# Kernel optimization log

Measured on AMD Instinct MI355X. Metric: run time of the kernel, lower is better.

The kernel has to match this reference:

```python
import jax, jax.numpy as jnp
import numpy as np

B, T, M, P = 256, 128, 64, 64


def setup_inputs() -> dict:
    key = jax.random.key(0)
    ks = jax.random.split(key, 20)
    s = 0.05
    inp = {
        "data": jax.random.normal(ks[0], (B, T - 1, 1), jnp.float32),
        "encoder_h": jax.random.normal(ks[1], (B, T, M), jnp.float32),
        "h0": jax.random.normal(ks[2], (B, P), jnp.float32),
        "s0": jax.random.normal(ks[3], (B, P), jnp.float32),
        # dense: Dense(1) on concat([x, context]) -> in=1+M
        "W_dense": jax.random.normal(ks[4], (1 + M, 1), jnp.float32) * s,
        "b_dense": jnp.zeros((1,), jnp.float32),
        # LSTM(p): kernel (1,4p), recurrent (p,4p), bias (4p); keras gate order i,f,c,o
        "Wk": jax.random.normal(ks[5], (1, 4 * P), jnp.float32) * s,
        "Uk": jax.random.normal(ks[6], (P, 4 * P), jnp.float32) * s,
        "bk": jnp.zeros((4 * P,), jnp.float32),
        # temporal attention: W_d Dense(m) on concat([h,c]) (2p -> m)
        "Wd": jax.random.normal(ks[7], (2 * P, M), jnp.float32) * s,
        "bWd": jnp.zeros((M,), jnp.float32),
        # U_d Dense(m) on encoder_h (m -> m)
        "Ud": jax.random.normal(ks[8], (M, M), jnp.float32) * s,
        "bUd": jnp.zeros((M,), jnp.float32),
        # v_d Dense(1)
        "vd": jax.random.normal(ks[9], (M, 1), jnp.float32) * s,
        "bvd": jnp.zeros((1,), jnp.float32),
        # dense_vb: Dense(1) on concat([h, context]) (p+m -> 1)
        "Wvb": jax.random.normal(ks[10], (P + M, 1), jnp.float32) * s,
        "bvb": jnp.zeros((1,), jnp.float32),
        # dense_Wb: Dense(p) applied AFTER dense_vb (1 -> p), as in the source
        "Wb": jax.random.normal(ks[11], (1, P), jnp.float32) * s,
        "bWb": jnp.zeros((P,), jnp.float32),
    }
    return inp


def reference(data, encoder_h, h0, s0, W_dense, b_dense, Wk, Uk, bk,
              Wd, bWd, Ud, bUd, vd, bvd, Wvb, bvb, Wb, bWb):
    # Loop-invariant: U_d(encoder_h), (B,T,M). Math identical to per-step compute.
    Ue = jnp.einsum('btm,mn->btn', encoder_h, Ud) + bUd

    def step(carry, x_t):
        ctx, _h = carry                      # ctx: (B,M)
        inp = jnp.concatenate([x_t, ctx], axis=-1)   # (B, 1+M)
        y = inp @ W_dense + b_dense                   # (B,1)
        # NOTE: source resets LSTM state to (h0, s0) at every step.
        z = y @ Wk + h0 @ Uk + bk                     # (B,4P)
        i_g, f_g, g_g, o_g = jnp.split(z, 4, axis=-1)
        c = jax.nn.sigmoid(f_g) * s0 + jax.nn.sigmoid(i_g) * jnp.tanh(g_g)
        h = jax.nn.sigmoid(o_g) * jnp.tanh(c)         # (B,P)
        # temporal attention
        dproj = jnp.concatenate([h, c], axis=-1) @ Wd + bWd   # (B,M)
        e = jnp.tanh(dproj[:, None, :] + Ue) @ vd + bvd        # (B,T,1)
        beta = jax.nn.softmax(e, axis=1)                       # (B,T,1)
        ctx_new = jnp.einsum('bti,btm->bm', beta, encoder_h)   # (B,M)
        return (ctx_new, h), None

    Bsz = encoder_h.shape[0]
    carry0 = (jnp.zeros((Bsz, Wk.shape[1] // 4 * 0 + encoder_h.shape[2]), encoder_h.dtype),
              jnp.zeros((Bsz, Uk.shape[0]), encoder_h.dtype))
    xs = jnp.transpose(data, (1, 0, 2))  # (T-1, B, 1)
    (ctx, h), _ = jax.lax.scan(step, carry0, xs)

    concatenated = jnp.concatenate([h, ctx], axis=-1)[:, None, :]  # (B,1,P+M)
    out = (concatenated @ Wvb + bvb) @ Wb + bWb                     # (B,1,P)
    return out
```

## Files before the change

kernel.cpp:

```cpp
#include <hip/hip_runtime.h>


#define Bn 256
#define Tn 128
#define Mn 64
#define Pn 64
#define NTH 512
#define NW 8
#define UST 68
#define DPST 72
#define K2C 2.885390081777927f

__device__ __forceinline__ float fexp(float x) {
    return __builtin_amdgcn_exp2f(x * 1.44269504088896341f);
}
__device__ __forceinline__ float fexp2(float x) { return __builtin_amdgcn_exp2f(x); }
__device__ __forceinline__ float frcp(float x) { return __builtin_amdgcn_rcpf(x); }
__device__ __forceinline__ float fsig(float x) { return frcp(1.0f + fexp(-x)); }
__device__ __forceinline__ float ftanh(float x) { return 1.0f - 2.0f * frcp(1.0f + fexp(2.0f * x)); }

template <int CTRL>
__device__ __forceinline__ float dppmov(float x) {
    return __int_as_float(__builtin_amdgcn_update_dpp(
        0, __float_as_int(x), CTRL, 0xf, 0xf, false));
}
__device__ __forceinline__ float rdlane(float x, int l) {
    return __int_as_float(__builtin_amdgcn_readlane(__float_as_int(x), l));
}
__device__ __forceinline__ float wavesum(float x) {
    x += dppmov<0x111>(x);
    x += dppmov<0x112>(x);
    x += dppmov<0x114>(x);
    x += dppmov<0x118>(x);
    x += dppmov<0x142>(x);
    x += dppmov<0x143>(x);
    return rdlane(x, 63);
}

#define OFF_ENC   0
#define OFF_UD    8704
#define OFF_PRE   13056
#define OFF_DPART 13312
#define OFF_DPROJ 13888
#define OFF_ES    13952
#define OFF_CTXP  14080
#define OFF_YS    14592
#define OFF_XS    14600
#define SMEM_FLOATS 14728

__global__ __launch_bounds__(NTH, 1)
void decoder_kernel(const float* __restrict__ data, const float* __restrict__ enc,
                    const float* __restrict__ h0, const float* __restrict__ s0,
                    const float* __restrict__ W_dense, const float* __restrict__ b_dense,
                    const float* __restrict__ Wk, const float* __restrict__ Uk,
                    const float* __restrict__ bk,
                    const float* __restrict__ Wd, const float* __restrict__ bWd,
                    const float* __restrict__ Ud, const float* __restrict__ bUd,
                    const float* __restrict__ vd, const float* __restrict__ bvd,
                    const float* __restrict__ Wvb, const float* __restrict__ bvb,
                    const float* __restrict__ Wb, const float* __restrict__ bWb,
                    float* __restrict__ out)
{
    extern __shared__ float smem[];
    float* enc_s   = smem + OFF_ENC;
    float* Ud_s    = smem + OFF_UD;
    float* pre_s   = smem + OFF_PRE;
    float* dpart   = smem + OFF_DPART;
    float* dproj_s = smem + OFF_DPROJ;
    float* e_s     = smem + OFF_ES;
    float* ctxp    = smem + OFF_CTXP;
    float* ys_s    = smem + OFF_YS;
    float* x_s     = smem + OFF_XS;

    const int b    = blockIdx.x;
    const int tid  = threadIdx.x;
    const int lane = tid & 63;
    const int wv   = tid >> 6;

    {
        const float* encg = enc + (size_t)b * Tn * Mn;
        #pragma unroll
        for (int i = 0; i < 4; i++) {
            int flat = (i * NTH + tid) * 4;
            int t = flat >> 6, m = flat & 63;
            *(float4*)(enc_s + t * UST + m) = *(const float4*)(encg + flat);
        }
        #pragma unroll
        for (int i = 0; i < 2; i++) {
            int flat = (i * NTH + tid) * 4;
            int k = flat >> 6, n = flat & 63;
            *(float4*)(Ud_s + k * UST + n) = *(const float4*)(Ud + flat);
        }
        if (tid < Tn - 1) x_s[tid] = data[(size_t)b * (Tn - 1) + tid];
        if (tid < 4 * Pn) {
            float s = bk[tid];
            const float* h0b = h0 + b * Pn;
            #pragma unroll
            for (int k = 0; k < Pn; k++) s = fmaf(h0b[k], Uk[k * 4 * Pn + tid], s);
            pre_s[tid] = s;
        }
        if (tid < NW) ys_s[tid] = 0.0f;
        ctxp[tid] = 0.0f;
    }
    __syncthreads();

    const int t_e = tid >> 2, q_e = tid & 3, m0 = q_e * 16;
    float ue_r[16];
    {
        float acc[16];
        #pragma unroll
        for (int j = 0; j < 16; j++) acc[j] = bUd[m0 + j];
        for (int k = 0; k < Mn; k++) {
            float a = enc_s[t_e * UST + k];
            const float4* ud = (const float4*)(Ud_s + k * UST + m0);
            #pragma unroll
            for (int j4 = 0; j4 < 4; j4++) {
                float4 u = ud[j4];
                acc[4 * j4 + 0] = fmaf(a, u.x, acc[4 * j4 + 0]);
                acc[4 * j4 + 1] = fmaf(a, u.y, acc[4 * j4 + 1]);
                acc[4 * j4 + 2] = fmaf(a, u.z, acc[4 * j4 + 2]);
                acc[4 * j4 + 3] = fmaf(a, u.w, acc[4 * j4 + 3]);
            }
        }
        #pragma unroll
        for (int j = 0; j < 16; j++) ue_r[j] = K2C * acc[j];
    }

    float enc_r[16], wd_r[16];
    #pragma unroll
    for (int j = 0; j < 16; j++) {
        enc_r[j] = enc_s[(16 * wv + j) * UST + lane];
        wd_r[j]  = Wd[(16 * wv + j) * Mn + lane];
    }
    const float W0  = W_dense[0];
    const float bd  = b_dense[0];
    const float Wde = W_dense[1 + lane];
    const float wk_i = Wk[lane], wk_f = Wk[64 + lane],
                wk_g = Wk[128 + lane], wk_o = Wk[192 + lane];
    const float s0v   = s0[b * Pn + lane];
    const float bvd0  = bvd[0];
    const float bwd_r = bWd[8 * wv + (lane >> 3)];
    float vdr2[16];
    float sumvd16 = 0.0f;
    #pragma unroll
    for (int j = 0; j < 16; j++) {
        float v = vd[m0 + j];
        vdr2[j] = -2.0f * v;
        sumvd16 += v;
    }
    const float pre_i = pre_s[lane];
    const float pre_f = pre_s[64 + lane];
    const float pre_g = pre_s[128 + lane];
    const float pre_o = pre_s[192 + lane];
    const bool hv_sel = (wv < 4);
    const int  base16 = (wv & 3) * 16;

    float h = 0.0f, c = 0.0f;

    for (int st = 0; st < Tn - 1; ++st) {
        float yv = ys_s[lane & 7];
        yv += dppmov<0x111>(yv);
        yv += dppmov<0x112>(yv);
        yv += dppmov<0x114>(yv);
        float y = fmaf(x_s[st], W0, rdlane(yv, 7) + bd);

        float zi = fmaf(y, wk_i, pre_i);
        float zf = fmaf(y, wk_f, pre_f);
        float zg = fmaf(y, wk_g, pre_g);
        float zo = fmaf(y, wk_o, pre_o);
        c = fsig(zf) * s0v + fsig(zi) * ftanh(zg);
        h = fsig(zo) * ftanh(c);

        {
            float hv = hv_sel ? h : c;
            float p0 = 0.0f, p1 = 0.0f, p2 = 0.0f, p3 = 0.0f;
            #pragma unroll
            for (int j = 0; j < 4; j++) {
                p0 = fmaf(rdlane(hv, base16 + j),      wd_r[j],      p0);
                p1 = fmaf(rdlane(hv, base16 + 4 + j),  wd_r[4 + j],  p1);
                p2 = fmaf(rdlane(hv, base16 + 8 + j),  wd_r[8 + j],  p2);
                p3 = fmaf(rdlane(hv, base16 + 12 + j), wd_r[12 + j], p3);
            }
            dpart[wv * DPST + lane] = (p0 + p1) + (p2 + p3);
        }
        __syncthreads();

        {
            int w  = lane & 7;
            int mi = lane >> 3;
            float v = dpart[w * DPST + 8 * wv + mi];
            v += dppmov<0x111>(v);
            v += dppmov<0x112>(v);
            v += dppmov<0x114>(v);
            if ((lane & 7) == 7) dproj_s[8 * wv + mi] = K2C * (v + bwd_r);
        }
        __syncthreads();

        {
            const float4* dp4 = (const float4*)(dproj_s + m0);
            float4 d0 = dp4[0], d1 = dp4[1], d2 = dp4[2], d3 = dp4[3];
            float a0 = sumvd16, a1 = 0.0f, a2 = 0.0f, a3 = 0.0f;
            a0 = fmaf(vdr2[0],  frcp(1.0f + fexp2(d0.x + ue_r[0])),  a0);
            a1 = fmaf(vdr2[1],  frcp(1.0f + fexp2(d0.y + ue_r[1])),  a1);
            a2 = fmaf(vdr2[2],  frcp(1.0f + fexp2(d0.z + ue_r[2])),  a2);
            a3 = fmaf(vdr2[3],  frcp(1.0f + fexp2(d0.w + ue_r[3])),  a3);
            a0 = fmaf(vdr2[4],  frcp(1.0f + fexp2(d1.x + ue_r[4])),  a0);
            a1 = fmaf(vdr2[5],  frcp(1.0f + fexp2(d1.y + ue_r[5])),  a1);
            a2 = fmaf(vdr2[6],  frcp(1.0f + fexp2(d1.z + ue_r[6])),  a2);
            a3 = fmaf(vdr2[7],  frcp(1.0f + fexp2(d1.w + ue_r[7])),  a3);
            a0 = fmaf(vdr2[8],  frcp(1.0f + fexp2(d2.x + ue_r[8])),  a0);
            a1 = fmaf(vdr2[9],  frcp(1.0f + fexp2(d2.y + ue_r[9])),  a1);
            a2 = fmaf(vdr2[10], frcp(1.0f + fexp2(d2.z + ue_r[10])), a2);
            a3 = fmaf(vdr2[11], frcp(1.0f + fexp2(d2.w + ue_r[11])), a3);
            a0 = fmaf(vdr2[12], frcp(1.0f + fexp2(d3.x + ue_r[12])), a0);
            a1 = fmaf(vdr2[13], frcp(1.0f + fexp2(d3.y + ue_r[13])), a1);
            a2 = fmaf(vdr2[14], frcp(1.0f + fexp2(d3.z + ue_r[14])), a2);
            a3 = fmaf(vdr2[15], frcp(1.0f + fexp2(d3.w + ue_r[15])), a3);
            float acc = (a0 + a1) + (a2 + a3);
            acc += dppmov<0x111>(acc);
            acc += dppmov<0x112>(acc);
            if (q_e == 3) e_s[t_e] = fexp(acc + bvd0);
        }
        __syncthreads();

        {
            float ex0 = e_s[lane];
            float ex1 = e_s[64 + lane];
            float invS = frcp(wavesum(ex0 + ex1));
            float exv = hv_sel ? ex0 : ex1;
            float p0 = 0.0f, p1 = 0.0f, p2 = 0.0f, p3 = 0.0f;
            #pragma unroll
            for (int j = 0; j < 4; j++) {
                p0 = fmaf(rdlane(exv, base16 + j),      enc_r[j],      p0);
                p1 = fmaf(rdlane(exv, base16 + 4 + j),  enc_r[4 + j],  p1);
                p2 = fmaf(rdlane(exv, base16 + 8 + j),  enc_r[8 + j],  p2);
                p3 = fmaf(rdlane(exv, base16 + 12 + j), enc_r[12 + j], p3);
            }
            float ctxv = ((p0 + p1) + (p2 + p3)) * invS;
            ctxp[wv * 64 + lane] = ctxv;
            float yw = ctxv * Wde;
            yw += dppmov<0x111>(yw);
            yw += dppmov<0x112>(yw);
            yw += dppmov<0x114>(yw);
            yw += dppmov<0x118>(yw);
            yw += dppmov<0x142>(yw);
            yw += dppmov<0x143>(yw);
            if (lane == 63) ys_s[wv] = yw;
        }
        __syncthreads();
    }

    if (wv == 0) {
        float ctxm = 0.0f;
        #pragma unroll
        for (int w = 0; w < NW; w++) ctxm += ctxp[w * 64 + lane];
        float part = h * Wvb[lane] + ctxm * Wvb[64 + lane];
        float v = wavesum(part) + bvb[0];
        out[(size_t)b * Pn + lane] = fmaf(v, Wb[lane], bWb[lane]);
    }
}

extern "C" void kernel_launch(void* const* d_in, const int* in_sizes, int n_in,
                              void* d_out, int out_size, void* d_ws, size_t ws_size,
                              hipStream_t stream) {
    const float* data    = (const float*)d_in[0];
    const float* enc     = (const float*)d_in[1];
    const float* h0      = (const float*)d_in[2];
    const float* s0      = (const float*)d_in[3];
    const float* W_dense = (const float*)d_in[4];
    const float* b_dense = (const float*)d_in[5];
    const float* Wk      = (const float*)d_in[6];
    const float* Uk      = (const float*)d_in[7];
    const float* bk      = (const float*)d_in[8];
    const float* Wd      = (const float*)d_in[9];
    const float* bWd     = (const float*)d_in[10];
    const float* Ud      = (const float*)d_in[11];
    const float* bUd     = (const float*)d_in[12];
    const float* vd      = (const float*)d_in[13];
    const float* bvd     = (const float*)d_in[14];
    const float* Wvb     = (const float*)d_in[15];
    const float* bvb     = (const float*)d_in[16];
    const float* Wb      = (const float*)d_in[17];
    const float* bWb     = (const float*)d_in[18];

    decoder_kernel<<<Bn, NTH, SMEM_FLOATS * sizeof(float), stream>>>(
        data, enc, h0, s0, W_dense, b_dense, Wk, Uk, bk,
        Wd, bWd, Ud, bUd, vd, bvd, Wvb, bvb, Wb, bWb, (float*)d_out);
}
```

Baseline: 310.7 us.

## Replace cross-wave reductions with LDS atomics to drop a barrier per step

The per-step dproj reduction now uses LDS atomicAdd into a bias-initialized buffer instead of a partial array plus a separate reduction stage, which removes one __syncthreads per recurrence step. The softmax denominator and the y scalar are also accumulated with double-buffered atomics, so the e_s array and the cross-wave sums go away. Each wave reads its own exp values through readlane. The attention tanh loop uses 2-wide float vectors to allow packed FMA, and the x inputs come from registers via readlane. Float atomic accumulation order is nondeterministic, and the atomics can contend on the same addresses.

```diff
diff --git a/kernel.cpp b/kernel.cpp
--- a/kernel.cpp
+++ b/kernel.cpp
@@ -8,8 +8,9 @@
 #define NTH 512
 #define NW 8
 #define UST 68
-#define DPST 72
 #define K2C 2.885390081777927f
+
+typedef float f32x2 __attribute__((ext_vector_type(2)));
 
 __device__ __forceinline__ float fexp(float x) {
     return __builtin_amdgcn_exp2f(x * 1.44269504088896341f);
@@ -27,26 +28,24 @@
 __device__ __forceinline__ float rdlane(float x, int l) {
     return __int_as_float(__builtin_amdgcn_readlane(__float_as_int(x), l));
 }
-__device__ __forceinline__ float wavesum(float x) {
+__device__ __forceinline__ float wavesum63(float x) {
     x += dppmov<0x111>(x);
     x += dppmov<0x112>(x);
     x += dppmov<0x114>(x);
     x += dppmov<0x118>(x);
     x += dppmov<0x142>(x);
     x += dppmov<0x143>(x);
-    return rdlane(x, 63);
+    return x;
 }
 
 #define OFF_ENC   0
 #define OFF_UD    8704
 #define OFF_PRE   13056
-#define OFF_DPART 13312
-#define OFF_DPROJ 13888
-#define OFF_ES    13952
-#define OFF_CTXP  14080
-#define OFF_YS    14592
-#define OFF_XS    14600
-#define SMEM_FLOATS 14728
+#define OFF_DPROJ 13312
+#define OFF_DEN   13376
+#define OFF_YS    13378
+#define OFF_CTXP  13380
+#define SMEM_FLOATS 13892
 
 __global__ __launch_bounds__(NTH, 1)
 void decoder_kernel(const float* __restrict__ data, const float* __restrict__ enc,
@@ -65,12 +64,10 @@
     float* enc_s   = smem + OFF_ENC;
     float* Ud_s    = smem + OFF_UD;
     float* pre_s   = smem + OFF_PRE;
-    float* dpart   = smem + OFF_DPART;
     float* dproj_s = smem + OFF_DPROJ;
-    float* e_s     = smem + OFF_ES;
+    float* den_s   = smem + OFF_DEN;
+    float* ys_s    = smem + OFF_YS;
     float* ctxp    = smem + OFF_CTXP;
-    float* ys_s    = smem + OFF_YS;
-    float* x_s     = smem + OFF_XS;
 
     const int b    = blockIdx.x;
     const int tid  = threadIdx.x;
@@ -91,7 +88,6 @@
             int k = flat >> 6, n = flat & 63;
             *(float4*)(Ud_s + k * UST + n) = *(const float4*)(Ud + flat);
         }
-        if (tid < Tn - 1) x_s[tid] = data[(size_t)b * (Tn - 1) + tid];
         if (tid < 4 * Pn) {
             float s = bk[tid];
             const float* h0b = h0 + b * Pn;
@@ -99,13 +95,13 @@
             for (int k = 0; k < Pn; k++) s = fmaf(h0b[k], Uk[k * 4 * Pn + tid], s);
             pre_s[tid] = s;
         }
-        if (tid < NW) ys_s[tid] = 0.0f;
-        ctxp[tid] = 0.0f;
+        if (tid < 64) dproj_s[tid] = K2C * bWd[tid];
+        if (tid < 2) { den_s[tid] = 0.0f; ys_s[tid] = 0.0f; }
     }
     __syncthreads();
 
     const int t_e = tid >> 2, q_e = tid & 3, m0 = q_e * 16;
-    float ue_r[16];
+    f32x2 ue2[8];
     {
         float acc[16];
         #pragma unroll
@@ -123,14 +119,17 @@
             }
         }
         #pragma unroll
-        for (int j = 0; j < 16; j++) ue_r[j] = K2C * acc[j];
+        for (int j = 0; j < 8; j++) {
+            ue2[j].x = K2C * acc[2 * j];
+            ue2[j].y = K2C * acc[2 * j + 1];
+        }
     }
 
     float enc_r[16], wd_r[16];
     #pragma unroll
     for (int j = 0; j < 16; j++) {
         enc_r[j] = enc_s[(16 * wv + j) * UST + lane];
-        wd_r[j]  = Wd[(16 * wv + j) * Mn + lane];
+        wd_r[j]  = K2C * Wd[(16 * wv + j) * Mn + lane];
     }
     const float W0  = W_dense[0];
     const float bd  = b_dense[0];
@@ -139,14 +138,14 @@
                 wk_g = Wk[128 + lane], wk_o = Wk[192 + lane];
     const float s0v   = s0[b * Pn + lane];
     const float bvd0  = bvd[0];
-    const float bwd_r = bWd[8 * wv + (lane >> 3)];
-    float vdr2[16];
+    const float bwd_pre = K2C * bWd[lane];
+    f32x2 vd2[8];
     float sumvd16 = 0.0f;
     #pragma unroll
-    for (int j = 0; j < 16; j++) {
-        float v = vd[m0 + j];
-        vdr2[j] = -2.0f * v;
-        sumvd16 += v;
+    for (int j = 0; j < 8; j++) {
+        float va = vd[m0 + 2 * j], vb = vd[m0 + 2 * j + 1];
+        vd2[j].x = -2.0f * va; vd2[j].y = -2.0f * vb;
+        sumvd16 += va + vb;
     }
     const float pre_i = pre_s[lane];
     const float pre_f = pre_s[64 + lane];
@@ -154,15 +153,18 @@
     const float pre_o = pre_s[192 + lane];
     const bool hv_sel = (wv < 4);
     const int  base16 = (wv & 3) * 16;
+    const float* xb = data + (size_t)b * (Tn - 1);
+    const float x_lo = xb[lane];
+    const float x_hi = (lane < 63) ? xb[64 + lane] : 0.0f;
 
     float h = 0.0f, c = 0.0f;
 
     for (int st = 0; st < Tn - 1; ++st) {
-        float yv = ys_s[lane & 7];
-        yv += dppmov<0x111>(yv);
-        yv += dppmov<0x112>(yv);
-        yv += dppmov<0x114>(yv);
-        float y = fmaf(x_s[st], W0, rdlane(yv, 7) + bd);
+        const int par = st & 1, nxt = par ^ 1;
+
+        float ysv = ys_s[par];
+        float xs = (st < 64) ? rdlane(x_lo, st) : rdlane(x_hi, st - 64);
+        float y = fmaf(xs, W0, ysv + bd);
 
         float zi = fmaf(y, wk_i, pre_i);
         float zf = fmaf(y, wk_f, pre_f);
@@ -181,71 +183,69 @@
                 p2 = fmaf(rdlane(hv, base16 + 8 + j),  wd_r[8 + j],  p2);
                 p3 = fmaf(rdlane(hv, base16 + 12 + j), wd_r[12 + j], p3);
             }
-            dpart[wv * DPST + lane] = (p0 + p1) + (p2 + p3);
+            atomicAdd(&dproj_s[lane], (p0 + p1) + (p2 + p3));
         }
         __syncthreads();
 
-        {
-            int w  = lane & 7;
-            int mi = lane >> 3;
-            float v = dpart[w * DPST + 8 * wv + mi];
-            v += dppmov<0x111>(v);
-            v += dppmov<0x112>(v);
-            v += dppmov<0x114>(v);
-            if ((lane & 7) == 7) dproj_s[8 * wv + mi] = K2C * (v + bwd_r);
-        }
-        __syncthreads();
-
+        float ex;
         {
             const float4* dp4 = (const float4*)(dproj_s + m0);
             float4 d0 = dp4[0], d1 = dp4[1], d2 = dp4[2], d3 = dp4[3];
-            float a0 = sumvd16, a1 = 0.0f, a2 = 0.0f, a3 = 0.0f;
-            a0 = fmaf(vdr2[0],  frcp(1.0f + fexp2(d0.x + ue_r[0])),  a0);
-            a1 = fmaf(vdr2[1],  frcp(1.0f + fexp2(d0.y + ue_r[1])),  a1);
-            a2 = fmaf(vdr2[2],  frcp(1.0f + fexp2(d0.z + ue_r[2])),  a2);
-            a3 = fmaf(vdr2[3],  frcp(1.0f + fexp2(d0.w + ue_r[3])),  a3);
-            a0 = fmaf(vdr2[4],  frcp(1.0f + fexp2(d1.x + ue_r[4])),  a0);
-            a1 = fmaf(vdr2[5],  frcp(1.0f + fexp2(d1.y + ue_r[5])),  a1);
-            a2 = fmaf(vdr2[6],  frcp(1.0f + fexp2(d1.z + ue_r[6])),  a2);
-            a3 = fmaf(vdr2[7],  frcp(1.0f + fexp2(d1.w + ue_r[7])),  a3);
-            a0 = fmaf(vdr2[8],  frcp(1.0f + fexp2(d2.x + ue_r[8])),  a0);
-            a1 = fmaf(vdr2[9],  frcp(1.0f + fexp2(d2.y + ue_r[9])),  a1);
-            a2 = fmaf(vdr2[10], frcp(1.0f + fexp2(d2.z + ue_r[10])), a2);
-            a3 = fmaf(vdr2[11], frcp(1.0f + fexp2(d2.w + ue_r[11])), a3);
-            a0 = fmaf(vdr2[12], frcp(1.0f + fexp2(d3.x + ue_r[12])), a0);
-            a1 = fmaf(vdr2[13], frcp(1.0f + fexp2(d3.y + ue_r[13])), a1);
-            a2 = fmaf(vdr2[14], frcp(1.0f + fexp2(d3.z + ue_r[14])), a2);
-            a3 = fmaf(vdr2[15], frcp(1.0f + fexp2(d3.w + ue_r[15])), a3);
-            float acc = (a0 + a1) + (a2 + a3);
+            f32x2 accA; accA.x = sumvd16; accA.y = 0.0f;
+            f32x2 accB; accB.x = 0.0f;    accB.y = 0.0f;
+            f32x2 s, r;
+            s.x = d0.x + ue2[0].x; s.y = d0.y + ue2[0].y;
+            r.x = frcp(1.0f + fexp2(s.x)); r.y = frcp(1.0f + fexp2(s.y));
+            accA += vd2[0] * r;
+            s.x = d0.z + ue2[1].x; s.y = d0.w + ue2[1].y;
+            r.x = frcp(1.0f + fexp2(s.x)); r.y = frcp(1.0f + fexp2(s.y));
+            accB += vd2[1] * r;
+            s.x = d1.x + ue2[2].x; s.y = d1.y + ue2[2].y;
+            r.x = frcp(1.0f + fexp2(s.x)); r.y = frcp(1.0f + fexp2(s.y));
+            accA += vd2[2] * r;
+            s.x = d1.z + ue2[3].x; s.y = d1.w + ue2[3].y;
+            r.x = frcp(1.0f + fexp2(s.x)); r.y = frcp(1.0f + fexp2(s.y));
+            accB += vd2[3] * r;
+            s.x = d2.x + ue2[4].x; s.y = d2.y + ue2[4].y;
+            r.x = frcp(1.0f + fexp2(s.x)); r.y = frcp(1.0f + fexp2(s.y));
+            accA += vd2[4] * r;
+            s.x = d2.z + ue2[5].x; s.y = d2.w + ue2[5].y;
+            r.x = frcp(1.0f + fexp2(s.x)); r.y = frcp(1.0f + fexp2(s.y));
+            accB += vd2[5] * r;
+            s.x = d3.x + ue2[6].x; s.y = d3.y + ue2[6].y;
+            r.x = frcp(1.0f + fexp2(s.x)); r.y = frcp(1.0f + fexp2(s.y));
+            accA += vd2[6] * r;
+            s.x = d3.z + ue2[7].x; s.y = d3.w + ue2[7].y;
+            r.x = frcp(1.0f + fexp2(s.x)); r.y = frcp(1.0f + fexp2(s.y));
+            accB += vd2[7] * r;
+            f32x2 accT = accA + accB;
+            float acc = accT.x + accT.y;
             acc += dppmov<0x111>(acc);
             acc += dppmov<0x112>(acc);
-            if (q_e == 3) e_s[t_e] = fexp(acc + bvd0);
+            ex = fexp(acc + bvd0);
+            float exm = (q_e == 3) ? ex : 0.0f;
+            float dsum = wavesum63(exm);
+            if (lane == 63) atomicAdd(&den_s[par], dsum);
         }
         __syncthreads();
 
         {
-            float ex0 = e_s[lane];
-            float ex1 = e_s[64 + lane];
-            float invS = frcp(wavesum(ex0 + ex1));
-            float exv = hv_sel ? ex0 : ex1;
+            float invS = frcp(den_s[par]);
             float p0 = 0.0f, p1 = 0.0f, p2 = 0.0f, p3 = 0.0f;
             #pragma unroll
             for (int j = 0; j < 4; j++) {
-                p0 = fmaf(rdlane(exv, base16 + j),      enc_r[j],      p0);
-                p1 = fmaf(rdlane(exv, base16 + 4 + j),  enc_r[4 + j],  p1);
-                p2 = fmaf(rdlane(exv, base16 + 8 + j),  enc_r[8 + j],  p2);
-                p3 = fmaf(rdlane(exv, base16 + 12 + j), enc_r[12 + j], p3);
+                p0 = fmaf(rdlane(ex, 4 * j + 3),        enc_r[j],      p0);
+                p1 = fmaf(rdlane(ex, 4 * (j + 4) + 3),  enc_r[4 + j],  p1);
+                p2 = fmaf(rdlane(ex, 4 * (j + 8) + 3),  enc_r[8 + j],  p2);
+                p3 = fmaf(rdlane(ex, 4 * (j + 12) + 3), enc_r[12 + j], p3);
             }
             float ctxv = ((p0 + p1) + (p2 + p3)) * invS;
-            ctxp[wv * 64 + lane] = ctxv;
-            float yw = ctxv * Wde;
-            yw += dppmov<0x111>(yw);
-            yw += dppmov<0x112>(yw);
-            yw += dppmov<0x114>(yw);
-            yw += dppmov<0x118>(yw);
-            yw += dppmov<0x142>(yw);
-            yw += dppmov<0x143>(yw);
-            if (lane == 63) ys_s[wv] = yw;
+            float yw = wavesum63(ctxv * Wde);
+            if (lane == 63) atomicAdd(&ys_s[nxt], yw);
+            if (tid == 0) ys_s[par] = 0.0f;
+            if (tid == 1) den_s[nxt] = 0.0f;
+            if (wv == 0) dproj_s[lane] = bwd_pre;
+            if (st == Tn - 2) ctxp[wv * 64 + lane] = ctxv;
         }
         __syncthreads();
     }
@@ -255,7 +255,7 @@
         #pragma unroll
         for (int w = 0; w < NW; w++) ctxm += ctxp[w * 64 + lane];
         float part = h * Wvb[lane] + ctxm * Wvb[64 + lane];
-        float v = wavesum(part) + bvb[0];
+        float v = rdlane(wavesum63(part), 63) + bvb[0];
         out[(size_t)b * Pn + lane] = fmaf(v, Wb[lane], bWb[lane]);
     }
 }
```

Result: slower. 364.9 us (+17.4%).
